# Kernel optimization log

Hardware: AMD Instinct MI355X
Metric: run time of the kernel (lower is better)

The kernel has to match this reference:

```python
import jax, jax.numpy as jnp
import numpy as np

N_NODES = 50000
N_EDGES = 1600000
D = 128


def setup_inputs() -> dict:
    key = jax.random.key(0)
    k1, k2, k3, k4 = jax.random.split(key, 4)
    x = jax.random.normal(k1, (N_NODES, D), dtype=jnp.float32)
    edge_index = jax.random.randint(k2, (2, N_EDGES), 0, N_NODES, dtype=jnp.int64)
    # Xavier-uniform-like W; B is zeros in torch init but use small random for grad coverage
    limit = float(np.sqrt(6.0 / (D + D)))
    W = jax.random.uniform(k3, (D, D), dtype=jnp.float32, minval=-limit, maxval=limit)
    B = jax.random.uniform(k4, (D, D), dtype=jnp.float32, minval=-limit, maxval=limit)
    return {"x": x, "edge_index": edge_index, "W": W, "B": B}


def reference(x, edge_index, W, B):
    sources = edge_index[0]
    destinations = edge_index[1]
    # gather messages from source nodes, scatter-add into destinations
    messages = x[sources]  # [E, D]
    aggregated = jax.ops.segment_sum(messages, destinations, num_segments=N_NODES)  # [N, D]
    deg = jax.ops.segment_sum(jnp.ones((N_EDGES,), dtype=x.dtype), destinations, num_segments=N_NODES)
    deg = jnp.where(deg == 0, jnp.asarray(1.0, dtype=x.dtype), deg)
    mean_msg = aggregated / deg[:, None]
    # update: messages @ W.T + x @ B.T
    return mean_msg @ W.T + x @ B.T
```

## Files before the change

kernel.cpp:

```cpp
#include <hip/hip_runtime.h>
#include <hip/hip_bf16.h>

#define NN 50000
#define NE 1600000
#define DD 128
#define NPB 64
#define NBK 782
#define SMAX 3072
#define CHUNK 3072
#define NCB 521
#define OTS 784
#define WS 136

typedef __attribute__((ext_vector_type(8))) short short8;
typedef __attribute__((ext_vector_type(4))) float f32x4;

__device__ inline unsigned short to_bf16(float v) {
    __hip_bfloat16 h = __float2bfloat16(v);
    return __builtin_bit_cast(unsigned short, h);
}
__device__ inline float bf2f(unsigned short u) {
    return __uint_as_float((unsigned)u << 16);
}

__global__ __launch_bounds__(1024) void convscatter_k(const int* __restrict__ ei,
                                                      const float* __restrict__ x,
                                                      const float* __restrict__ W,
                                                      const float* __restrict__ Bm,
                                                      unsigned int* __restrict__ xb,
                                                      unsigned short* __restrict__ Wbf,
                                                      unsigned short* __restrict__ Bbf,
                                                      int* __restrict__ ebuf,
                                                      unsigned short* __restrict__ offtab) {
    __shared__ int stg[CHUNK];
    __shared__ int h[NBK];
    __shared__ int lbase[NBK];
    __shared__ int hcur[NBK];
    __shared__ int wsum[16], wbase[16];
    const int t = threadIdx.x;
    const int lane = t & 63, wv = t >> 6;
    const int e0 = blockIdx.x * CHUNK;
    const int ec = min(CHUNK, NE - e0);

    for (int i = t; i < NBK; i += 1024) h[i] = 0;
    __syncthreads();

    unsigned int w2[3];
    #pragma unroll
    for (int u = 0; u < 3; ++u) {
        int i = u * 1024 + t;
        if (i < ec) {
            int src = ei[e0 + i];
            int dst = ei[NE + e0 + i];
            int b = dst >> 6;
            w2[u] = ((unsigned)b << 22) | ((unsigned)src << 6) | (unsigned)(dst & 63);
            atomicAdd(&h[b], 1);
        } else w2[u] = 0xFFFFFFFFu;
    }

    {
        int gid = blockIdx.x * 1024 + t;
        const int total4 = NN * DD / 4;
        for (int i = gid; i < total4; i += NCB * 1024) {
            float4 v = ((const float4*)x)[i];
            int p = __builtin_amdgcn_cvt_pk_fp8_f32(v.x, v.y, 0, false);
            p = __builtin_amdgcn_cvt_pk_fp8_f32(v.z, v.w, p, true);
            xb[i] = (unsigned)p;
        }
    }
    if (blockIdx.x == NCB - 1) {
        for (int i = t; i < DD * DD / 4; i += 1024) {
            float4 w4 = ((const float4*)W)[i];
            float4 b4 = ((const float4*)Bm)[i];
            ushort4 wp, bp;
            wp.x = to_bf16(w4.x); wp.y = to_bf16(w4.y); wp.z = to_bf16(w4.z); wp.w = to_bf16(w4.w);
            bp.x = to_bf16(b4.x); bp.y = to_bf16(b4.y); bp.z = to_bf16(b4.z); bp.w = to_bf16(b4.w);
            ((ushort4*)Wbf)[i] = wp;
            ((ushort4*)Bbf)[i] = bp;
        }
    }
    __syncthreads();

    int v = (t < NBK) ? h[t] : 0;
    int s = v;
    #pragma unroll
    for (int o = 1; o < 64; o <<= 1) {
        int u = __shfl_up(s, o);
        if (lane >= o) s += u;
    }
    if (lane == 63) wsum[wv] = s;
    __syncthreads();
    if (wv == 0 && lane < 16) {
        int bv = wsum[lane];
        int bs = bv;
        #pragma unroll
        for (int o = 1; o < 16; o <<= 1) {
            int u = __shfl_up(bs, o);
            if (lane >= o) bs += u;
        }
        wbase[lane] = bs - bv;
    }
    __syncthreads();
    if (t < NBK) {
        int excl = s - v + wbase[wv];
        lbase[t] = excl;
        hcur[t] = excl;
    }
    __syncthreads();

    for (int i = t; i <= NBK; i += 1024)
        offtab[(size_t)blockIdx.x * OTS + i] = (unsigned short)((i < NBK) ? lbase[i] : ec);

    #pragma unroll
    for (int u = 0; u < 3; ++u) {
        if (w2[u] != 0xFFFFFFFFu) {
            int b = w2[u] >> 22;
            int pos = atomicAdd(&hcur[b], 1);
            stg[pos] = (int)(w2[u] & 0x3FFFFFu);
        }
    }
    __syncthreads();

    for (int i = t; i < (ec >> 2); i += 1024)
        ((int4*)(ebuf + e0))[i] = ((const int4*)stg)[i];
}

#define ACC2(U)                                                              \
    {                                                                        \
        auto l0 = __builtin_amdgcn_cvt_pk_f32_fp8((int)(U).x, false);        \
        auto h0 = __builtin_amdgcn_cvt_pk_f32_fp8((int)(U).x, true);         \
        auto l1 = __builtin_amdgcn_cvt_pk_f32_fp8((int)(U).y, false);        \
        auto h1 = __builtin_amdgcn_cvt_pk_f32_fp8((int)(U).y, true);         \
        a0 += l0[0]; a1 += l0[1]; a2 += h0[0]; a3 += h0[1];                  \
        a4 += l1[0]; a5 += l1[1]; a6 += h1[0]; a7 += h1[1];                  \
    }

__global__ __launch_bounds__(1024) void sortagg_k(const unsigned int* __restrict__ xb,
                                                  const int* __restrict__ ebuf,
                                                  const unsigned short* __restrict__ offtab,
                                                  unsigned short* __restrict__ psb,
                                                  unsigned short* __restrict__ pcnt) {
    __shared__ int stg[SMAX];
    __shared__ unsigned short srt[SMAX];
    __shared__ int cnt16[16][NPB];
    __shared__ int cur[NPB], off[NPB + 1];
    __shared__ int segoff[NCB + 1];
    __shared__ int srcb[NCB];
    __shared__ int ws16[16], wb16[16];
    const int b = blockIdx.x, t = threadIdx.x;
    const int wv = t >> 6, lane = t & 63;

    int v = 0;
    if (t < NCB) {
        int o1 = offtab[(size_t)t * OTS + b];
        int o2 = offtab[(size_t)t * OTS + b + 1];
        v = o2 - o1;
        srcb[t] = t * CHUNK + o1;
    }
    int s = v;
    #pragma unroll
    for (int o = 1; o < 64; o <<= 1) {
        int u = __shfl_up(s, o);
        if (lane >= o) s += u;
    }
    if (lane == 63) ws16[wv] = s;
    cnt16[wv][lane] = 0;
    __syncthreads();
    if (wv == 0 && lane < 16) {
        int bv = ws16[lane], bs = bv;
        #pragma unroll
        for (int o = 1; o < 16; o <<= 1) {
            int u = __shfl_up(bs, o);
            if (lane >= o) bs += u;
        }
        wb16[lane] = bs - bv;
    }
    __syncthreads();
    int excl = s - v + wb16[wv];
    if (t < NCB) segoff[t] = excl;
    if (t == NCB - 1) segoff[NCB] = excl + v;
    __syncthreads();
    const int n = min(segoff[NCB], SMAX);

    for (int i = t; i < n; i += 1024) {
        int lo = 0, hi = NCB - 1;
        #pragma unroll
        for (int it = 0; it < 10; ++it) {
            int mid = (lo + hi + 1) >> 1;
            if (segoff[mid] <= i) lo = mid; else hi = mid - 1;
        }
        int val = ebuf[srcb[lo] + (i - segoff[lo])];
        stg[i] = val;
        atomicAdd(&cnt16[wv][val & 63], 1);
    }
    __syncthreads();

    if (t < 64) {
        int vv = 0;
        #pragma unroll
        for (int w = 0; w < 16; ++w) vv += cnt16[w][t];
        int ss = vv;
        #pragma unroll
        for (int o = 1; o < 64; o <<= 1) {
            int u = __shfl_up(ss, o);
            if (t >= o) ss += u;
        }
        cur[t] = ss - vv;
        off[t] = ss - vv;
        if (t == 63) off[64] = ss;
    }
    __syncthreads();
    for (int i = t; i < n; i += 1024) {
        int w = stg[i];
        int pos = atomicAdd(&cur[w & 63], 1);
        srt[pos] = (unsigned short)(w >> 6);
    }
    __syncthreads();

    const int sub = lane >> 4, il2 = lane & 15;
    #pragma unroll
    for (int q = 0; q < 4; ++q) {
        int ln = wv + q * 16;
        int s0 = off[ln], s1 = off[ln + 1];
        float a0 = 0.f, a1 = 0.f, a2 = 0.f, a3 = 0.f;
        float a4 = 0.f, a5 = 0.f, a6 = 0.f, a7 = 0.f;
        int i = s0;
        for (; i + 16 <= s1; i += 16) {
            uint2 u[4];
            #pragma unroll
            for (int k = 0; k < 4; ++k)
                u[k] = ((const uint2*)xb)[(size_t)srt[i + 4 * k + sub] * 16 + il2];
            #pragma unroll
            for (int k = 0; k < 4; ++k) ACC2(u[k]);
        }
        if (i < s1) {
            uint2 u[4];
            #pragma unroll
            for (int k = 0; k < 4; ++k) {
                int e = i + 4 * k + sub;
                if (e < s1) u[k] = ((const uint2*)xb)[(size_t)srt[e] * 16 + il2];
                else { u[k].x = 0u; u[k].y = 0u; }
            }
            #pragma unroll
            for (int k = 0; k < 4; ++k) ACC2(u[k]);
        }
        a0 += __shfl_xor(a0, 16); a0 += __shfl_xor(a0, 32);
        a1 += __shfl_xor(a1, 16); a1 += __shfl_xor(a1, 32);
        a2 += __shfl_xor(a2, 16); a2 += __shfl_xor(a2, 32);
        a3 += __shfl_xor(a3, 16); a3 += __shfl_xor(a3, 32);
        a4 += __shfl_xor(a4, 16); a4 += __shfl_xor(a4, 32);
        a5 += __shfl_xor(a5, 16); a5 += __shfl_xor(a5, 32);
        a6 += __shfl_xor(a6, 16); a6 += __shfl_xor(a6, 32);
        a7 += __shfl_xor(a7, 16); a7 += __shfl_xor(a7, 32);
        int node = b * NPB + ln;
        if (node < NN) {
            if (lane < 16) {
                short8 sv;
                sv[0] = (short)to_bf16(a0); sv[1] = (short)to_bf16(a1);
                sv[2] = (short)to_bf16(a2); sv[3] = (short)to_bf16(a3);
                sv[4] = (short)to_bf16(a4); sv[5] = (short)to_bf16(a5);
                sv[6] = (short)to_bf16(a6); sv[7] = (short)to_bf16(a7);
                *(short8*)&psb[(size_t)node * DD + il2 * 8] = sv;
            }
            if (lane == 0) pcnt[node] = (unsigned short)(s1 - s0);
        }
    }
}

__global__ __launch_bounds__(512) void gemm_mfma_k(const unsigned short* __restrict__ psb,
                                                   const unsigned short* __restrict__ pcnt,
                                                   const float* __restrict__ x,
                                                   const unsigned short* __restrict__ Wbf,
                                                   const unsigned short* __restrict__ Bbf,
                                                   float* __restrict__ out) {
    __shared__ unsigned short Wt[DD * WS];
    __shared__ unsigned short Bt[DD * WS];
    const int tid = threadIdx.x;
    #pragma unroll
    for (int it = 0; it < 8; ++it) {
        int idx = it * 512 + tid;
        int n = idx >> 5;
        int k0 = (idx & 31) * 4;
        *(ushort4*)&Wt[n * WS + k0] = ((const ushort4*)Wbf)[idx];
        *(ushort4*)&Bt[n * WS + k0] = ((const ushort4*)Bbf)[idx];
    }
    __syncthreads();

    const int wave = tid >> 6;
    const int lane = tid & 63;
    const int m = lane & 15;
    const int quad = lane >> 4;
    const int rowA = min(blockIdx.x * 128 + wave * 16 + m, NN - 1);

    const float deg = (float)pcnt[rowA];
    const float inv = 1.0f / fmaxf(deg, 1.0f);

    f32x4 acc[8];
    #pragma unroll
    for (int nt = 0; nt < 8; ++nt) acc[nt] = (f32x4){0.f, 0.f, 0.f, 0.f};

    #pragma unroll
    for (int t = 0; t < 4; ++t) {
        const int k8 = t * 32 + quad * 8;
        short8 p0 = *(const short8*)&psb[(size_t)rowA * DD + k8];
        short8 mf;
        #pragma unroll
        for (int j = 0; j < 8; ++j)
            mf[j] = (short)to_bf16(bf2f((unsigned short)p0[j]) * inv);

        float xv[8];
        {
            const float4* xq = (const float4*)&x[(size_t)rowA * DD + k8];
            float4 b0 = xq[0], b1 = xq[1];
            xv[0] = b0.x; xv[1] = b0.y; xv[2] = b0.z; xv[3] = b0.w;
            xv[4] = b1.x; xv[5] = b1.y; xv[6] = b1.z; xv[7] = b1.w;
        }
        short8 xh, xl;
        #pragma unroll
        for (int j = 0; j < 8; ++j) {
            unsigned short g = to_bf16(xv[j]);
            xh[j] = (short)g;
            xl[j] = (short)to_bf16(xv[j] - __uint_as_float((unsigned)g << 16));
        }
        #pragma unroll
        for (int nt = 0; nt < 8; ++nt) {
            int nrow = nt * 16 + m;
            short8 wf = *(const short8*)&Wt[nrow * WS + k8];
            short8 bf = *(const short8*)&Bt[nrow * WS + k8];
            acc[nt] = __builtin_amdgcn_mfma_f32_16x16x32_bf16(xl, bf, acc[nt], 0, 0, 0);
            acc[nt] = __builtin_amdgcn_mfma_f32_16x16x32_bf16(mf, wf, acc[nt], 0, 0, 0);
            acc[nt] = __builtin_amdgcn_mfma_f32_16x16x32_bf16(xh, bf, acc[nt], 0, 0, 0);
        }
    }

    const int rowD0 = blockIdx.x * 128 + wave * 16 + quad * 4;
    #pragma unroll
    for (int nt = 0; nt < 8; ++nt) {
        #pragma unroll
        for (int r = 0; r < 4; ++r) {
            int row = rowD0 + r;
            if (row < NN) out[(size_t)row * DD + nt * 16 + m] = acc[nt][r];
        }
    }
}

extern "C" void kernel_launch(void* const* d_in, const int* in_sizes, int n_in,
                              void* d_out, int out_size, void* d_ws, size_t ws_size,
                              hipStream_t stream) {
    const float* x  = (const float*)d_in[0];
    const int*   ei = (const int*)d_in[1];
    const float* W  = (const float*)d_in[2];
    const float* Bm = (const float*)d_in[3];
    float* out = (float*)d_out;

    unsigned int* xb      = (unsigned int*)d_ws;
    int* ebuf             = (int*)(xb + (size_t)NN * 32);
    unsigned short* offtab= (unsigned short*)(ebuf + (size_t)NE);
    unsigned short* Wbf   = offtab + (size_t)NCB * OTS;
    unsigned short* Bbf   = Wbf + DD * DD;
    unsigned short* psb   = Bbf + DD * DD;
    unsigned short* pcnt  = psb + (size_t)NN * DD;

    convscatter_k<<<NCB, 1024, 0, stream>>>(ei, x, W, Bm, xb, Wbf, Bbf, ebuf, offtab);
    sortagg_k<<<NBK, 1024, 0, stream>>>(xb, ebuf, offtab, psb, pcnt);
    gemm_mfma_k<<<(NN + 127) / 128, 512, 0, stream>>>(psb, pcnt, x, Wbf, Bbf, out);
}
```

Before: 141.9 us.

## Split edges into smaller chunks and make sort-aggregate a persistent atomic work queue

The edge-bucketing kernel now runs a fixed grid of 512 blocks, each handling two chunks of 1568 edges instead of one chunk of 3072. The sort-aggregate kernel becomes persistent: 512 blocks pull destination-bucket indices from a global atomic counter (reset by the first kernel) rather than launching one block per bucket. The aim is better load balance and fewer tail waves across CUs. In exchange, each bucket must now read and binary-search twice as many offset segments (1021 vs 521), and every bucket fetch costs an extra atomic and barrier.

```diff
diff --git a/kernel.cpp b/kernel.cpp
--- a/kernel.cpp
+++ b/kernel.cpp
@@ -7,9 +7,10 @@
 #define NPB 64
 #define NBK 782
 #define SMAX 3072
-#define CHUNK 3072
-#define NCB 521
-#define OTS 784
+#define CHUNK 1568
+#define NSEG 1021
+#define OTS 1024
+#define CGRID 512
 #define WS 136
 
 typedef __attribute__((ext_vector_type(8))) short short8;
@@ -31,7 +32,8 @@
                                                       unsigned short* __restrict__ Wbf,
                                                       unsigned short* __restrict__ Bbf,
                                                       int* __restrict__ ebuf,
-                                                      unsigned short* __restrict__ offtab) {
+                                                      unsigned short* __restrict__ offtab,
+                                                      int* __restrict__ qctl) {
     __shared__ int stg[CHUNK];
     __shared__ int h[NBK];
     __shared__ int lbase[NBK];
@@ -39,36 +41,20 @@
     __shared__ int wsum[16], wbase[16];
     const int t = threadIdx.x;
     const int lane = t & 63, wv = t >> 6;
-    const int e0 = blockIdx.x * CHUNK;
-    const int ec = min(CHUNK, NE - e0);
-
-    for (int i = t; i < NBK; i += 1024) h[i] = 0;
-    __syncthreads();
-
-    unsigned int w2[3];
-    #pragma unroll
-    for (int u = 0; u < 3; ++u) {
-        int i = u * 1024 + t;
-        if (i < ec) {
-            int src = ei[e0 + i];
-            int dst = ei[NE + e0 + i];
-            int b = dst >> 6;
-            w2[u] = ((unsigned)b << 22) | ((unsigned)src << 6) | (unsigned)(dst & 63);
-            atomicAdd(&h[b], 1);
-        } else w2[u] = 0xFFFFFFFFu;
-    }
+
+    if (blockIdx.x == 0 && t == 0) qctl[0] = 0;
 
     {
         int gid = blockIdx.x * 1024 + t;
         const int total4 = NN * DD / 4;
-        for (int i = gid; i < total4; i += NCB * 1024) {
+        for (int i = gid; i < total4; i += CGRID * 1024) {
             float4 v = ((const float4*)x)[i];
             int p = __builtin_amdgcn_cvt_pk_fp8_f32(v.x, v.y, 0, false);
             p = __builtin_amdgcn_cvt_pk_fp8_f32(v.z, v.w, p, true);
             xb[i] = (unsigned)p;
         }
     }
-    if (blockIdx.x == NCB - 1) {
+    if (blockIdx.x == CGRID - 1) {
         for (int i = t; i < DD * DD / 4; i += 1024) {
             float4 w4 = ((const float4*)W)[i];
             float4 b4 = ((const float4*)Bm)[i];
@@ -79,50 +65,75 @@
             ((ushort4*)Bbf)[i] = bp;
         }
     }
-    __syncthreads();
-
-    int v = (t < NBK) ? h[t] : 0;
-    int s = v;
-    #pragma unroll
-    for (int o = 1; o < 64; o <<= 1) {
-        int u = __shfl_up(s, o);
-        if (lane >= o) s += u;
-    }
-    if (lane == 63) wsum[wv] = s;
-    __syncthreads();
-    if (wv == 0 && lane < 16) {
-        int bv = wsum[lane];
-        int bs = bv;
-        #pragma unroll
-        for (int o = 1; o < 16; o <<= 1) {
-            int u = __shfl_up(bs, o);
-            if (lane >= o) bs += u;
-        }
-        wbase[lane] = bs - bv;
-    }
-    __syncthreads();
-    if (t < NBK) {
-        int excl = s - v + wbase[wv];
-        lbase[t] = excl;
-        hcur[t] = excl;
-    }
-    __syncthreads();
-
-    for (int i = t; i <= NBK; i += 1024)
-        offtab[(size_t)blockIdx.x * OTS + i] = (unsigned short)((i < NBK) ? lbase[i] : ec);
-
-    #pragma unroll
-    for (int u = 0; u < 3; ++u) {
-        if (w2[u] != 0xFFFFFFFFu) {
-            int b = w2[u] >> 22;
-            int pos = atomicAdd(&hcur[b], 1);
-            stg[pos] = (int)(w2[u] & 0x3FFFFFu);
-        }
-    }
-    __syncthreads();
-
-    for (int i = t; i < (ec >> 2); i += 1024)
-        ((int4*)(ebuf + e0))[i] = ((const int4*)stg)[i];
+
+    #pragma unroll 1
+    for (int rep = 0; rep < 2; ++rep) {
+        const int c = blockIdx.x + rep * CGRID;
+        const int e0 = c * CHUNK;
+        const int ec = min(CHUNK, NE - e0);
+        if (ec <= 0) break;
+
+        for (int i = t; i < NBK; i += 1024) h[i] = 0;
+        __syncthreads();
+
+        unsigned int w2[2];
+        #pragma unroll
+        for (int u = 0; u < 2; ++u) {
+            int i = u * 1024 + t;
+            if (i < ec) {
+                int src = ei[e0 + i];
+                int dst = ei[NE + e0 + i];
+                int b = dst >> 6;
+                w2[u] = ((unsigned)b << 22) | ((unsigned)src << 6) | (unsigned)(dst & 63);
+                atomicAdd(&h[b], 1);
+            } else w2[u] = 0xFFFFFFFFu;
+        }
+        __syncthreads();
+
+        int v = (t < NBK) ? h[t] : 0;
+        int s = v;
+        #pragma unroll
+        for (int o = 1; o < 64; o <<= 1) {
+            int u = __shfl_up(s, o);
+            if (lane >= o) s += u;
+        }
+        if (lane == 63) wsum[wv] = s;
+        __syncthreads();
+        if (wv == 0 && lane < 16) {
+            int bv = wsum[lane];
+            int bs = bv;
+            #pragma unroll
+            for (int o = 1; o < 16; o <<= 1) {
+                int u = __shfl_up(bs, o);
+                if (lane >= o) bs += u;
+            }
+            wbase[lane] = bs - bv;
+        }
+        __syncthreads();
+        if (t < NBK) {
+            int excl = s - v + wbase[wv];
+            lbase[t] = excl;
+            hcur[t] = excl;
+        }
+        __syncthreads();
+
+        for (int i = t; i <= NBK; i += 1024)
+            offtab[(size_t)c * OTS + i] = (unsigned short)((i < NBK) ? lbase[i] : ec);
+
+        #pragma unroll
+        for (int u = 0; u < 2; ++u) {
+            if (w2[u] != 0xFFFFFFFFu) {
+                int b = w2[u] >> 22;
+                int pos = atomicAdd(&hcur[b], 1);
+                stg[pos] = (int)(w2[u] & 0x3FFFFFu);
+            }
+        }
+        __syncthreads();
+
+        for (int i = t; i < (ec >> 2); i += 1024)
+            ((int4*)(ebuf + e0))[i] = ((const int4*)stg)[i];
+        __syncthreads();
+    }
 }
 
 #define ACC2(U)                                                              \
@@ -139,131 +150,141 @@
                                                   const int* __restrict__ ebuf,
                                                   const unsigned short* __restrict__ offtab,
                                                   unsigned short* __restrict__ psb,
-                                                  unsigned short* __restrict__ pcnt) {
+                                                  unsigned short* __restrict__ pcnt,
+                                                  int* __restrict__ qctl) {
     __shared__ int stg[SMAX];
     __shared__ unsigned short srt[SMAX];
     __shared__ int cnt16[16][NPB];
     __shared__ int cur[NPB], off[NPB + 1];
-    __shared__ int segoff[NCB + 1];
-    __shared__ int srcb[NCB];
+    __shared__ int segoff[NSEG + 1];
+    __shared__ int srcb[NSEG];
     __shared__ int ws16[16], wb16[16];
-    const int b = blockIdx.x, t = threadIdx.x;
+    __shared__ int sh_b;
+    const int t = threadIdx.x;
     const int wv = t >> 6, lane = t & 63;
-
-    int v = 0;
-    if (t < NCB) {
-        int o1 = offtab[(size_t)t * OTS + b];
-        int o2 = offtab[(size_t)t * OTS + b + 1];
-        v = o2 - o1;
-        srcb[t] = t * CHUNK + o1;
-    }
-    int s = v;
-    #pragma unroll
-    for (int o = 1; o < 64; o <<= 1) {
-        int u = __shfl_up(s, o);
-        if (lane >= o) s += u;
-    }
-    if (lane == 63) ws16[wv] = s;
-    cnt16[wv][lane] = 0;
-    __syncthreads();
-    if (wv == 0 && lane < 16) {
-        int bv = ws16[lane], bs = bv;
-        #pragma unroll
-        for (int o = 1; o < 16; o <<= 1) {
-            int u = __shfl_up(bs, o);
-            if (lane >= o) bs += u;
-        }
-        wb16[lane] = bs - bv;
-    }
-    __syncthreads();
-    int excl = s - v + wb16[wv];
-    if (t < NCB) segoff[t] = excl;
-    if (t == NCB - 1) segoff[NCB] = excl + v;
-    __syncthreads();
-    const int n = min(segoff[NCB], SMAX);
-
-    for (int i = t; i < n; i += 1024) {
-        int lo = 0, hi = NCB - 1;
-        #pragma unroll
-        for (int it = 0; it < 10; ++it) {
-            int mid = (lo + hi + 1) >> 1;
-            if (segoff[mid] <= i) lo = mid; else hi = mid - 1;
-        }
-        int val = ebuf[srcb[lo] + (i - segoff[lo])];
-        stg[i] = val;
-        atomicAdd(&cnt16[wv][val & 63], 1);
-    }
-    __syncthreads();
-
-    if (t < 64) {
-        int vv = 0;
-        #pragma unroll
-        for (int w = 0; w < 16; ++w) vv += cnt16[w][t];
-        int ss = vv;
+    const int sub = lane >> 4, il2 = lane & 15;
+
+    for (;;) {
+        if (t == 0) sh_b = atomicAdd(&qctl[0], 1);
+        __syncthreads();
+        const int b = sh_b;
+        if (b >= NBK) break;
+
+        int v = 0;
+        if (t < NSEG) {
+            int o1 = offtab[(size_t)t * OTS + b];
+            int o2 = offtab[(size_t)t * OTS + b + 1];
+            v = o2 - o1;
+            srcb[t] = t * CHUNK + o1;
+        }
+        int s = v;
         #pragma unroll
         for (int o = 1; o < 64; o <<= 1) {
-            int u = __shfl_up(ss, o);
-            if (t >= o) ss += u;
-        }
-        cur[t] = ss - vv;
-        off[t] = ss - vv;
-        if (t == 63) off[64] = ss;
-    }
-    __syncthreads();
-    for (int i = t; i < n; i += 1024) {
-        int w = stg[i];
-        int pos = atomicAdd(&cur[w & 63], 1);
-        srt[pos] = (unsigned short)(w >> 6);
-    }
-    __syncthreads();
-
-    const int sub = lane >> 4, il2 = lane & 15;
-    #pragma unroll
-    for (int q = 0; q < 4; ++q) {
-        int ln = wv + q * 16;
-        int s0 = off[ln], s1 = off[ln + 1];
-        float a0 = 0.f, a1 = 0.f, a2 = 0.f, a3 = 0.f;
-        float a4 = 0.f, a5 = 0.f, a6 = 0.f, a7 = 0.f;
-        int i = s0;
-        for (; i + 16 <= s1; i += 16) {
-            uint2 u[4];
-            #pragma unroll
-            for (int k = 0; k < 4; ++k)
-                u[k] = ((const uint2*)xb)[(size_t)srt[i + 4 * k + sub] * 16 + il2];
-            #pragma unroll
-            for (int k = 0; k < 4; ++k) ACC2(u[k]);
-        }
-        if (i < s1) {
-            uint2 u[4];
-            #pragma unroll
-            for (int k = 0; k < 4; ++k) {
-                int e = i + 4 * k + sub;
-                if (e < s1) u[k] = ((const uint2*)xb)[(size_t)srt[e] * 16 + il2];
-                else { u[k].x = 0u; u[k].y = 0u; }
-            }
-            #pragma unroll
-            for (int k = 0; k < 4; ++k) ACC2(u[k]);
-        }
-        a0 += __shfl_xor(a0, 16); a0 += __shfl_xor(a0, 32);
-        a1 += __shfl_xor(a1, 16); a1 += __shfl_xor(a1, 32);
-        a2 += __shfl_xor(a2, 16); a2 += __shfl_xor(a2, 32);
-        a3 += __shfl_xor(a3, 16); a3 += __shfl_xor(a3, 32);
-        a4 += __shfl_xor(a4, 16); a4 += __shfl_xor(a4, 32);
-        a5 += __shfl_xor(a5, 16); a5 += __shfl_xor(a5, 32);
-        a6 += __shfl_xor(a6, 16); a6 += __shfl_xor(a6, 32);
-        a7 += __shfl_xor(a7, 16); a7 += __shfl_xor(a7, 32);
-        int node = b * NPB + ln;
-        if (node < NN) {
-            if (lane < 16) {
-                short8 sv;
-                sv[0] = (short)to_bf16(a0); sv[1] = (short)to_bf16(a1);
-                sv[2] = (short)to_bf16(a2); sv[3] = (short)to_bf16(a3);
-                sv[4] = (short)to_bf16(a4); sv[5] = (short)to_bf16(a5);
-                sv[6] = (short)to_bf16(a6); sv[7] = (short)to_bf16(a7);
-                *(short8*)&psb[(size_t)node * DD + il2 * 8] = sv;
-            }
-            if (lane == 0) pcnt[node] = (unsigned short)(s1 - s0);
-        }
+            int u = __shfl_up(s, o);
+            if (lane >= o) s += u;
+        }
+        if (lane == 63) ws16[wv] = s;
+        cnt16[wv][lane] = 0;
+        __syncthreads();
+        if (wv == 0 && lane < 16) {
+            int bv = ws16[lane], bs = bv;
+            #pragma unroll
+            for (int o = 1; o < 16; o <<= 1) {
+                int u = __shfl_up(bs, o);
+                if (lane >= o) bs += u;
+            }
+            wb16[lane] = bs - bv;
+        }
+        __syncthreads();
+        int excl = s - v + wb16[wv];
+        if (t < NSEG) segoff[t] = excl;
+        if (t == NSEG - 1) segoff[NSEG] = excl + v;
+        __syncthreads();
+        const int n = min(segoff[NSEG], SMAX);
+
+        for (int i = t; i < n; i += 1024) {
+            int lo = 0, hi = NSEG - 1;
+            #pragma unroll
+            for (int it = 0; it < 10; ++it) {
+                int mid = (lo + hi + 1) >> 1;
+                if (segoff[mid] <= i) lo = mid; else hi = mid - 1;
+            }
+            int val = ebuf[srcb[lo] + (i - segoff[lo])];
+            stg[i] = val;
+            atomicAdd(&cnt16[wv][val & 63], 1);
+        }
+        __syncthreads();
+
+        if (t < 64) {
+            int vv = 0;
+            #pragma unroll
+            for (int w = 0; w < 16; ++w) vv += cnt16[w][t];
+            int ss = vv;
+            #pragma unroll
+            for (int o = 1; o < 64; o <<= 1) {
+                int u = __shfl_up(ss, o);
+                if (t >= o) ss += u;
+            }
+            cur[t] = ss - vv;
+            off[t] = ss - vv;
+            if (t == 63) off[64] = ss;
+        }
+        __syncthreads();
+        for (int i = t; i < n; i += 1024) {
+            int w = stg[i];
+            int pos = atomicAdd(&cur[w & 63], 1);
+            srt[pos] = (unsigned short)(w >> 6);
+        }
+        __syncthreads();
+
+        #pragma unroll
+        for (int q = 0; q < 4; ++q) {
+            int ln = wv + q * 16;
+            int s0 = off[ln], s1 = off[ln + 1];
+            float a0 = 0.f, a1 = 0.f, a2 = 0.f, a3 = 0.f;
+            float a4 = 0.f, a5 = 0.f, a6 = 0.f, a7 = 0.f;
+            int i = s0;
+            for (; i + 16 <= s1; i += 16) {
+                uint2 u[4];
+                #pragma unroll
+                for (int k = 0; k < 4; ++k)
+                    u[k] = ((const uint2*)xb)[(size_t)srt[i + 4 * k + sub] * 16 + il2];
+                #pragma unroll
+                for (int k = 0; k < 4; ++k) ACC2(u[k]);
+            }
+            if (i < s1) {
+                uint2 u[4];
+                #pragma unroll
+                for (int k = 0; k < 4; ++k) {
+                    int e = i + 4 * k + sub;
+                    if (e < s1) u[k] = ((const uint2*)xb)[(size_t)srt[e] * 16 + il2];
+                    else { u[k].x = 0u; u[k].y = 0u; }
+                }
+                #pragma unroll
+                for (int k = 0; k < 4; ++k) ACC2(u[k]);
+            }
+            a0 += __shfl_xor(a0, 16); a0 += __shfl_xor(a0, 32);
+            a1 += __shfl_xor(a1, 16); a1 += __shfl_xor(a1, 32);
+            a2 += __shfl_xor(a2, 16); a2 += __shfl_xor(a2, 32);
+            a3 += __shfl_xor(a3, 16); a3 += __shfl_xor(a3, 32);
+            a4 += __shfl_xor(a4, 16); a4 += __shfl_xor(a4, 32);
+            a5 += __shfl_xor(a5, 16); a5 += __shfl_xor(a5, 32);
+            a6 += __shfl_xor(a6, 16); a6 += __shfl_xor(a6, 32);
+            a7 += __shfl_xor(a7, 16); a7 += __shfl_xor(a7, 32);
+            int node = b * NPB + ln;
+            if (node < NN) {
+                if (lane < 16) {
+                    short8 sv;
+                    sv[0] = (short)to_bf16(a0); sv[1] = (short)to_bf16(a1);
+                    sv[2] = (short)to_bf16(a2); sv[3] = (short)to_bf16(a3);
+                    sv[4] = (short)to_bf16(a4); sv[5] = (short)to_bf16(a5);
+                    sv[6] = (short)to_bf16(a6); sv[7] = (short)to_bf16(a7);
+                    *(short8*)&psb[(size_t)node * DD + il2 * 8] = sv;
+                }
+                if (lane == 0) pcnt[node] = (unsigned short)(s1 - s0);
+            }
+        }
+        __syncthreads();
     }
 }
 
@@ -356,12 +377,13 @@
     unsigned int* xb      = (unsigned int*)d_ws;
     int* ebuf             = (int*)(xb + (size_t)NN * 32);
     unsigned short* offtab= (unsigned short*)(ebuf + (size_t)NE);
-    unsigned short* Wbf   = offtab + (size_t)NCB * OTS;
+    unsigned short* Wbf   = offtab + (size_t)NSEG * OTS;
     unsigned short* Bbf   = Wbf + DD * DD;
     unsigned short* psb   = Bbf + DD * DD;
     unsigned short* pcnt  = psb + (size_t)NN * DD;
-
-    convscatter_k<<<NCB, 1024, 0, stream>>>(ei, x, W, Bm, xb, Wbf, Bbf, ebuf, offtab);
-    sortagg_k<<<NBK, 1024, 0, stream>>>(xb, ebuf, offtab, psb, pcnt);
+    int* qctl             = (int*)(pcnt + (size_t)NN + (NN & 1));
+
+    convscatter_k<<<CGRID, 1024, 0, stream>>>(ei, x, W, Bm, xb, Wbf, Bbf, ebuf, offtab, qctl);
+    sortagg_k<<<512, 1024, 0, stream>>>(xb, ebuf, offtab, psb, pcnt, qctl);
     gemm_mfma_k<<<(NN + 127) / 128, 512, 0, stream>>>(psb, pcnt, x, Wbf, Bbf, out);
 }
```

After: 154.4 us. 8.8% more time.
